# Performance work log

Hardware: AMD Instinct MI355X
Metric: run time of the kernel (lower is better)

Reference implementation:

```python
import jax, jax.numpy as jnp
import numpy as np
from jax import lax

D_MODEL = 96; D_STATE = 16; D_INNER = 192; DT_RANK = 6; K = 4
BSZ = 2; HH = 64; WW = 64


def setup_inputs() -> dict:
    key = jax.random.key(0)
    ks = jax.random.split(key, 16)
    f = lambda k, shape, s=0.02: (jax.random.normal(k, shape) * s).astype(jnp.float32)
    P = DT_RANK + 2 * D_STATE
    return {
        "x": jax.random.normal(ks[0], (BSZ, HH, WW, D_MODEL), jnp.float32),
        "W_in": f(ks[1], (2 * D_INNER, D_MODEL)),
        "b_in": jnp.zeros((2 * D_INNER,), jnp.float32),
        "conv_w": f(ks[2], (D_INNER, 1, 3, 3)),
        "conv_b": jnp.zeros((D_INNER,), jnp.float32),
        "W_xp": f(ks[3], (K * P, K * D_INNER)),
        "b_xp": jnp.zeros((K * P,), jnp.float32),
        "W_dt": f(ks[4], (K * D_INNER, K * DT_RANK)),
        "b_dt": f(ks[5], (K * D_INNER,), 0.1),
        "A_log": jax.random.normal(ks[6], (K * D_INNER, D_STATE), jnp.float32),
        "D_skip": jnp.ones((K * D_INNER,), jnp.float32),
        "dt_bias": jax.random.normal(ks[7], (K * D_INNER,), jnp.float32),
        "W_out": f(ks[8], (D_MODEL, D_INNER)),
        "b_out": jnp.zeros((D_MODEL,), jnp.float32),
        "gamma": jnp.ones((D_INNER,), jnp.float32),
        "beta": jnp.zeros((D_INNER,), jnp.float32),
    }


def cross_scan(x):
    # x: (B, D, H, W) -> (B, 4, D, L); dirs: row-major, col-major, and their reverses
    B, D, H, W = x.shape
    L = H * W
    x0 = x.reshape(B, D, L)
    x1 = jnp.swapaxes(x, 2, 3).reshape(B, D, L)
    return jnp.stack([x0, x1, x0[..., ::-1], x1[..., ::-1]], axis=1)


def cross_merge(ys):
    # ys: (B, 4, D, H, W) -> (B, D, L); inverse of cross_scan, summed
    B, Kk, D, H, W = ys.shape
    L = H * W
    yf = ys.reshape(B, Kk, D, L)
    y02 = yf[:, 0] + yf[:, 2, :, ::-1]
    y13 = yf[:, 1] + yf[:, 3, :, ::-1]
    y13 = jnp.swapaxes(y13.reshape(B, D, W, H), 2, 3).reshape(B, D, L)
    return y02 + y13


def selective_scan(u, dt, A, Bm, Cm, D_skip, dt_bias):
    # u, dt: (B,K,Dv,L); A: (K,Dv,N); Bm, Cm: (B,K,N,L); D_skip, dt_bias: (K,Dv)
    # NOTE: torch code repeats Bm/Cm across Dv; we broadcast instead (same math).
    dt = jax.nn.softplus(dt + dt_bias[None, :, :, None])
    dt_l = jnp.moveaxis(dt, -1, 0)   # (L,B,K,Dv)
    u_l = jnp.moveaxis(u, -1, 0)     # (L,B,K,Dv)
    B_l = jnp.moveaxis(Bm, -1, 0)    # (L,B,K,N)
    C_l = jnp.moveaxis(Cm, -1, 0)    # (L,B,K,N)

    def step(h, inp):
        dt_t, u_t, b_t, c_t = inp
        dA = jnp.exp(dt_t[..., None] * A[None])                 # (B,K,Dv,N)
        dBu = (dt_t * u_t)[..., None] * b_t[:, :, None, :]      # (B,K,Dv,N)
        h = dA * h + dBu
        y = jnp.einsum('bkdn,bkn->bkd', h, c_t)
        return h, y

    h0 = jnp.zeros(u.shape[:3] + (A.shape[-1],), u.dtype)
    _, ys = lax.scan(step, h0, (dt_l, u_l, B_l, C_l))
    ys = jnp.moveaxis(ys, 0, -1)  # (B,K,Dv,L)
    return ys + u * D_skip[None, :, :, None]


def reference(x, W_in, b_in, conv_w, conv_b, W_xp, b_xp, W_dt, b_dt,
              A_log, D_skip, dt_bias, W_out, b_out, gamma, beta):
    B, H, W, _ = x.shape
    L = H * W
    xz = x @ W_in.T + b_in
    xx, z = jnp.split(xz, 2, axis=-1)
    z = jax.nn.silu(z)
    xc = jnp.transpose(xx, (0, 3, 1, 2))  # (B, D, H, W)
    xc = lax.conv_general_dilated(xc, conv_w, (1, 1), 'SAME',
                                  feature_group_count=D_INNER,
                                  dimension_numbers=('NCHW', 'OIHW', 'NCHW'))
    xc = jax.nn.silu(xc + conv_b[None, :, None, None])

    xs = cross_scan(xc)                      # (B, K, D, L)
    xs_flat = xs.reshape(B, K * D_INNER, L)

    x_dbl = jnp.einsum('bcl,pc->bpl', xs_flat, W_xp) + b_xp[None, :, None]
    x_dbl = x_dbl.reshape(B, K, DT_RANK + 2 * D_STATE, L)
    dts, Bm, Cm = jnp.split(x_dbl, [DT_RANK, DT_RANK + D_STATE], axis=2)
    dts = dts.reshape(B, K * DT_RANK, L)
    dts = jnp.einsum('brl,dr->bdl', dts, W_dt) + b_dt[None, :, None]

    A = -jnp.exp(A_log).reshape(K, D_INNER, D_STATE)
    u = xs_flat.reshape(B, K, D_INNER, L)
    dt = dts.reshape(B, K, D_INNER, L)
    ys = selective_scan(u, dt, A, Bm, Cm,
                        D_skip.reshape(K, D_INNER), dt_bias.reshape(K, D_INNER))

    y = cross_merge(ys.reshape(B, K, D_INNER, H, W))  # (B, D, L)
    y = jnp.transpose(y.reshape(B, D_INNER, H, W), (0, 2, 3, 1))

    mu = jnp.mean(y, axis=-1, keepdims=True)
    var = jnp.mean(jnp.square(y - mu), axis=-1, keepdims=True)
    y = (y - mu) * lax.rsqrt(var + 1e-5) * gamma + beta
    y = y * z
    return y @ W_out.T + b_out
```

## Files before the change

### kernel.cpp

```cpp
#include <hip/hip_runtime.h>
#include <cstdint>
#include <cstddef>


#define CHUNK 32
#define NCK   128

#if __has_builtin(__builtin_amdgcn_exp2f)
#define EXP2(x) __builtin_amdgcn_exp2f(x)
#else
#define EXP2(x) exp2f(x)
#endif
#define LOG2E 1.44269504088896340736f

typedef __attribute__((ext_vector_type(8))) short short8;
typedef __attribute__((ext_vector_type(8))) unsigned short ushort8;
typedef __attribute__((ext_vector_type(4))) float f32x4;

__device__ __forceinline__ float siluf(float x){ return x * (1.f/(1.f+__expf(-x))); }
__device__ __forceinline__ unsigned short f2b(float f){
  uint32_t u = __float_as_uint(f);
  uint32_t r = (u + 0x7fffu + ((u>>16)&1u)) >> 16;
  return (unsigned short)r;
}

template<int KD, int STRA, int STRB>
__device__ __forceinline__ void micro_mm_T(const float (&As)[64][STRA], const float (&BsT)[KD][STRB],
                                           int tx, int ty, float (&acc)[4][4])
{
#pragma unroll 2
  for (int k4 = 0; k4 < KD/4; k4++){
    float a[4][4];
#pragma unroll
    for (int i = 0; i < 4; i++){
      float4 t = *(const float4*)&As[ty*4+i][k4*4];
      a[i][0]=t.x; a[i][1]=t.y; a[i][2]=t.z; a[i][3]=t.w;
    }
#pragma unroll
    for (int e = 0; e < 4; e++){
      float4 b = *(const float4*)&BsT[k4*4+e][tx*4];
#pragma unroll
      for (int i = 0; i < 4; i++){
        acc[i][0] = fmaf(a[i][e], b.x, acc[i][0]);
        acc[i][1] = fmaf(a[i][e], b.y, acc[i][1]);
        acc[i][2] = fmaf(a[i][e], b.z, acc[i][2]);
        acc[i][3] = fmaf(a[i][e], b.w, acc[i][3]);
      }
    }
  }
}

__global__ __launch_bounds__(256) void k_cast_w(
    const float* __restrict__ Wxp, unsigned short* __restrict__ Wf)
{
  int tid = blockIdx.x*256 + threadIdx.x;
  if (tid >= 18432) return;
  int lane = tid & 63; int rest = tid >> 6;
  int pt = rest % 6; rest /= 6;
  int k32 = rest & 3; rest >>= 2;
  int kc = rest % 6; int ph = rest / 6;
  int n = lane & 15, q = lane >> 4;
  int p = ph*96 + pt*16 + n;
  int kbase = kc*128 + k32*32 + q*8;
  unsigned short v[8];
#pragma unroll
  for (int j = 0; j < 8; j++)
    v[j] = (p < 152) ? f2b(Wxp[(size_t)p*768 + kbase + j]) : (unsigned short)0;
  *(ushort8*)(Wf + (size_t)tid*8) = *(ushort8*)v;
}

__global__ __launch_bounds__(256) void k_gemm_in(
    const float* __restrict__ x, const float* __restrict__ W,
    const float* __restrict__ bias, float* __restrict__ xx, float* __restrict__ zs)
{
  __shared__ float As[64][100];
  __shared__ float BsT[96][68];
  const int m0 = blockIdx.x*64, n0 = blockIdx.y*64;
  const int tid = threadIdx.x;
#pragma unroll
  for (int i = 0; i < 6; i++){
    int idx = tid + i*256;
    { int r = idx/24, c4 = idx%24;
      *(float4*)&As[r][c4*4] = *(const float4*)(x + (size_t)(m0+r)*96 + c4*4); }
    { int r = idx & 63, c4 = idx >> 6;
      float4 wv = *(const float4*)(W + (size_t)(n0+r)*96 + c4*4);
      BsT[c4*4+0][r]=wv.x; BsT[c4*4+1][r]=wv.y; BsT[c4*4+2][r]=wv.z; BsT[c4*4+3][r]=wv.w; }
  }
  __syncthreads();
  const int tx = tid & 15, ty = tid >> 4;
  float acc[4][4] = {};
  micro_mm_T<96,100,68>(As, BsT, tx, ty, acc);
#pragma unroll
  for (int i = 0; i < 4; i++){
    int m = m0 + ty*4 + i;
#pragma unroll
    for (int j = 0; j < 4; j++){
      int n = n0 + tx*4 + j;
      float v = acc[i][j] + bias[n];
      if (n < 192) xx[(size_t)m*192 + n] = v;
      else         zs[(size_t)m*192 + (n-192)] = siluf(v);
    }
  }
}

__global__ __launch_bounds__(256) void k_conv(
    const float* __restrict__ xx, const float* __restrict__ cw, const float* __restrict__ cb,
    float* __restrict__ xc, float* __restrict__ xcT,
    unsigned short* __restrict__ xcb, unsigned short* __restrict__ xcTb)
{
  int gid = blockIdx.x*256 + threadIdx.x;
  int c = gid % 192;
  int l = (gid/192) & 4095;
  int b = gid / (192*4096);
  int h = l >> 6, w = l & 63;
  float s = 0.f;
#pragma unroll
  for (int kh = 0; kh < 3; kh++){
    int h2 = h + kh - 1;
    if ((unsigned)h2 >= 64u) continue;
#pragma unroll
    for (int kw = 0; kw < 3; kw++){
      int w2 = w + kw - 1;
      if ((unsigned)w2 >= 64u) continue;
      s += xx[((size_t)b*4096 + h2*64 + w2)*192 + c] * cw[c*9 + kh*3 + kw];
    }
  }
  s = siluf(s + cb[c]);
  unsigned short sb = f2b(s);
  size_t i0 = ((size_t)b*4096 + l)*192 + c;
  xc[i0] = s; xcb[i0] = sb;
  int tl = (l & 63)*64 + (l >> 6);
  size_t i1 = ((size_t)b*4096 + tl)*192 + c;
  xcT[i1] = s; xcTb[i1] = sb;
}

__global__ __launch_bounds__(256) void k_gemm_xdbl(
    const unsigned short* __restrict__ xcb, const unsigned short* __restrict__ xcTb,
    const unsigned short* __restrict__ Wf, const float* __restrict__ bxp,
    float* __restrict__ xdbl)
{
  __shared__ unsigned short Bsh[4*6*64*8];
  const int tid = threadIdx.x;
  const int lane = tid & 63, w = tid >> 6;
  const int wl = w & 1, wp = w >> 1;
  const int l0 = blockIdx.x*64, ph = blockIdx.y, b = blockIdx.z;
  const int n = lane & 15, q = lane >> 4;
  f32x4 acc[2][3] = {};
  const unsigned short* slab0 = Wf + (size_t)ph*6*12288;
  for (int kc = 0; kc < 6; kc++){
    __syncthreads();
    const ushort8* srcp = (const ushort8*)(slab0 + (size_t)kc*12288);
#pragma unroll
    for (int t = 0; t < 6; t++) ((ushort8*)Bsh)[tid + t*256] = srcp[tid + t*256];
    __syncthreads();
#pragma unroll
    for (int k32 = 0; k32 < 4; k32++){
      int kk = kc*128 + k32*32;
      int dir = kk/192; int ch = kk%192 + q*8;
      const unsigned short* sp = (dir & 1) ? xcTb : xcb;
      bool rev = (dir >= 2);
      short8 a[2];
#pragma unroll
      for (int mt = 0; mt < 2; mt++){
        int ls = l0 + wl*32 + mt*16 + n;
        int row = rev ? 4095 - ls : ls;
        a[mt] = *(const short8*)(sp + ((size_t)b*4096 + row)*192 + ch);
      }
#pragma unroll
      for (int j = 0; j < 3; j++){
        short8 bfr = *(const short8*)&Bsh[((size_t)(k32*6 + wp*3 + j)*64 + lane)*8];
#pragma unroll
        for (int mt = 0; mt < 2; mt++)
          acc[mt][j] = __builtin_amdgcn_mfma_f32_16x16x32_bf16(a[mt], bfr, acc[mt][j], 0, 0, 0);
      }
    }
  }
#pragma unroll
  for (int mt = 0; mt < 2; mt++)
#pragma unroll
    for (int j = 0; j < 3; j++){
      int p = ph*96 + (wp*3+j)*16 + n;
      if (p < 152){
        int k = p/38, pp = p%38;
        int off = (pp < 6) ? pp : pp + 2;
        float bias = bxp[p];
#pragma unroll
        for (int reg = 0; reg < 4; reg++){
          int l = l0 + wl*32 + mt*16 + q*4 + reg;
          xdbl[(((size_t)b*4 + k)*4096 + l)*48 + off] = acc[mt][j][reg] + bias;
        }
      }
    }
}

__global__ __launch_bounds__(256) void k_gemm_dt(
    const float* __restrict__ xdbl, const float* __restrict__ Wdt,
    const float* __restrict__ bdt, const float* __restrict__ dtbias,
    float* __restrict__ dte)
{
  __shared__ float As[64][28];
  __shared__ float BsT[24][68];
  const int m0 = blockIdx.x*64;
  const int n0 = blockIdx.y*64;
  const int b  = blockIdx.z;
  const int tid = threadIdx.x;
#pragma unroll
  for (int i = 0; i < 6; i++){
    int idx = tid + i*256;
    { int r = idx/24, cc = idx%24;
      int kp = cc/6, ri = cc%6;
      As[r][cc] = xdbl[(((size_t)b*4 + kp)*4096 + (m0+r))*48 + ri]; }
    { int r = idx & 63, cc = idx >> 6;
      BsT[cc][r] = Wdt[(size_t)(n0+r)*24 + cc]; }
  }
  __syncthreads();
  const int tx = tid & 15, ty = tid >> 4;
  float acc[4][4] = {};
  micro_mm_T<24,28,68>(As, BsT, tx, ty, acc);
#pragma unroll
  for (int i = 0; i < 4; i++){
    int l = m0 + ty*4 + i;
#pragma unroll
    for (int j = 0; j < 4; j++){
      int c = n0 + tx*4 + j;
      float v = acc[i][j] + bdt[c] + dtbias[c];
      v = (v > 20.f) ? v : log1pf(__expf(v));
      dte[(((size_t)b*4 + c/192)*4096 + l)*192 + (c%192)] = v;
    }
  }
}

__global__ __launch_bounds__(256) void k_scanA(
    const float* __restrict__ xc, const float* __restrict__ xcT,
    const float* __restrict__ xdbl, const float* __restrict__ dte,
    const float* __restrict__ A_log,
    float* __restrict__ Pb, float* __restrict__ Sb)
{
  const int lane = threadIdx.x & 63;
  const int wid  = __builtin_amdgcn_readfirstlane(blockIdx.x*4 + (threadIdx.x >> 6));
  const int ck = wid & (NCK-1); const int g = wid / NCK;
  const int dblk = g % 3; const int bk = g / 3;
  const int k = bk & 3; const int b = bk >> 2;
  const int d = dblk*64 + lane; const int ch = k*192 + d;
  float An[16];
  {
    const float4* ap = (const float4*)(A_log + (size_t)ch*16);
#pragma unroll
    for (int i = 0; i < 4; i++){
      float4 t = ap[i];
      An[4*i+0] = -LOG2E*__expf(t.x); An[4*i+1] = -LOG2E*__expf(t.y);
      An[4*i+2] = -LOG2E*__expf(t.z); An[4*i+3] = -LOG2E*__expf(t.w);
    }
  }
  const int l0 = ck*CHUNK;
  const bool rev = (k >= 2);
  const float* srcb = (k & 1) ? xcT : xc;
  const float* dtp = dte  + (((size_t)b*4 + k)*4096 + l0)*192 + d;
  const float* xdp = xdbl + (((size_t)b*4 + k)*4096 + l0)*48;
  const float* up  = srcb + ((size_t)b*4096 + (rev ? 4095 - l0 : l0))*192 + d;
  const int ust = rev ? -192 : 192;
  float h[16];
#pragma unroll
  for (int n = 0; n < 16; n++) h[n] = 0.f;
  float sdt = 0.f;
#pragma unroll 2
  for (int t = 0; t < CHUNK; t++){
    float dt = dtp[0];
    float u  = up[0];
    float4 B0 = *(const float4*)(xdp + 8);
    float4 B1 = *(const float4*)(xdp + 12);
    float4 B2 = *(const float4*)(xdp + 16);
    float4 B3 = *(const float4*)(xdp + 20);
    float Bv[16] = {B0.x,B0.y,B0.z,B0.w, B1.x,B1.y,B1.z,B1.w,
                    B2.x,B2.y,B2.z,B2.w, B3.x,B3.y,B3.z,B3.w};
    float dtu = dt*u;
    sdt += dt;
#pragma unroll
    for (int n = 0; n < 16; n++){
      float dA = EXP2(dt*An[n]);
      h[n] = fmaf(dA, h[n], dtu*Bv[n]);
    }
    dtp += 192; xdp += 48; up += ust;
  }
  size_t base = ((size_t)wid*16)*64 + lane;
#pragma unroll
  for (int n = 0; n < 16; n++){
    Pb[base + n*64] = EXP2(An[n]*sdt);
    Sb[base + n*64] = h[n];
  }
}

__global__ __launch_bounds__(256) void k_scanB(
    const float* __restrict__ Pb, float* SbH0)
{
  int tid = blockIdx.x*256 + threadIdx.x;
  int lane = tid & 63; int n = (tid >> 6) & 15; int g = tid >> 10;
  float h = 0.f;
  for (int ck = 0; ck < NCK; ck++){
    size_t idx = (((size_t)(g*NCK + ck)*16) + n)*64 + lane;
    float p = Pb[idx];
    float s = SbH0[idx];
    SbH0[idx] = h;
    h = fmaf(p, h, s);
  }
}

__global__ __launch_bounds__(256) void k_scanC(
    const float* __restrict__ xc, const float* __restrict__ xcT,
    const float* __restrict__ xdbl, const float* __restrict__ dte,
    const float* __restrict__ A_log, const float* __restrict__ Dskip,
    const float* __restrict__ H0, float* __restrict__ ys)
{
  const int lane = threadIdx.x & 63;
  const int wid  = __builtin_amdgcn_readfirstlane(blockIdx.x*4 + (threadIdx.x >> 6));
  const int ck = wid & (NCK-1); const int g = wid / NCK;
  const int dblk = g % 3; const int bk = g / 3;
  const int k = bk & 3; const int b = bk >> 2;
  const int d = dblk*64 + lane; const int ch = k*192 + d;
  float An[16];
  {
    const float4* ap = (const float4*)(A_log + (size_t)ch*16);
#pragma unroll
    for (int i = 0; i < 4; i++){
      float4 t = ap[i];
      An[4*i+0] = -LOG2E*__expf(t.x); An[4*i+1] = -LOG2E*__expf(t.y);
      An[4*i+2] = -LOG2E*__expf(t.z); An[4*i+3] = -LOG2E*__expf(t.w);
    }
  }
  const float Dv = Dskip[ch];
  const int l0 = ck*CHUNK;
  const bool rev = (k >= 2);
  const float* srcb = (k & 1) ? xcT : xc;
  const float* dtp = dte  + (((size_t)b*4 + k)*4096 + l0)*192 + d;
  const float* xdp = xdbl + (((size_t)b*4 + k)*4096 + l0)*48;
  const float* up  = srcb + ((size_t)b*4096 + (rev ? 4095 - l0 : l0))*192 + d;
  const int ust = rev ? -192 : 192;
  float* ysb = ys + ((size_t)(k*2 + b))*4096*192 + d;
  float h[16];
  size_t base = ((size_t)wid*16)*64 + lane;
#pragma unroll
  for (int n = 0; n < 16; n++) h[n] = H0[base + n*64];
#pragma unroll 2
  for (int t = 0; t < CHUNK; t++){
    int l = l0 + t;
    float dt = dtp[0];
    float u  = up[0];
    float4 B0 = *(const float4*)(xdp + 8);
    float4 B1 = *(const float4*)(xdp + 12);
    float4 B2 = *(const float4*)(xdp + 16);
    float4 B3 = *(const float4*)(xdp + 20);
    float4 C0 = *(const float4*)(xdp + 24);
    float4 C1 = *(const float4*)(xdp + 28);
    float4 C2 = *(const float4*)(xdp + 32);
    float4 C3 = *(const float4*)(xdp + 36);
    float Bv[16] = {B0.x,B0.y,B0.z,B0.w, B1.x,B1.y,B1.z,B1.w,
                    B2.x,B2.y,B2.z,B2.w, B3.x,B3.y,B3.z,B3.w};
    float Cv[16] = {C0.x,C0.y,C0.z,C0.w, C1.x,C1.y,C1.z,C1.w,
                    C2.x,C2.y,C2.z,C2.w, C3.x,C3.y,C3.z,C3.w};
    float dtu = dt*u;
    float y = u*Dv;
#pragma unroll
    for (int n = 0; n < 16; n++){
      float dA = EXP2(dt*An[n]);
      h[n] = fmaf(dA, h[n], dtu*Bv[n]);
      y = fmaf(h[n], Cv[n], y);
    }
    int pos;
    if (k == 0)      pos = l;
    else if (k == 1) pos = (l & 63)*64 + (l >> 6);
    else { int l2 = 4095 - l; pos = (k == 2) ? l2 : ((l2 & 63)*64 + (l2 >> 6)); }
    ysb[(size_t)pos*192] = y;
    dtp += 192; xdp += 48; up += ust;
  }
}

__global__ __launch_bounds__(256) void k_ln(
    const float* __restrict__ ys, const float* __restrict__ zs,
    const float* __restrict__ gamma, const float* __restrict__ beta,
    float* __restrict__ yln)
{
  int row = blockIdx.x*4 + (threadIdx.x >> 6);
  int lane = threadIdx.x & 63;
  int b = row >> 12; int l = row & 4095;
  float v[3];
#pragma unroll
  for (int j = 0; j < 3; j++){
    int c = lane + j*64;
    float s = 0.f;
#pragma unroll
    for (int k = 0; k < 4; k++) s += ys[(((size_t)k*2 + b)*4096 + l)*192 + c];
    v[j] = s;
  }
  float tot = v[0] + v[1] + v[2];
#pragma unroll
  for (int o = 1; o < 64; o <<= 1) tot += __shfl_xor(tot, o);
  float mean = tot * (1.f/192.f);
  float d0 = v[0]-mean, d1 = v[1]-mean, d2 = v[2]-mean;
  float vs = d0*d0 + d1*d1 + d2*d2;
#pragma unroll
  for (int o = 1; o < 64; o <<= 1) vs += __shfl_xor(vs, o);
  float rstd = rsqrtf(vs*(1.f/192.f) + 1e-5f);
  float nd[3] = {d0, d1, d2};
#pragma unroll
  for (int j = 0; j < 3; j++){
    int c = lane + j*64;
    float val = nd[j]*rstd*gamma[c] + beta[c];
    val *= zs[(size_t)row*192 + c];
    yln[(size_t)row*192 + c] = val;
  }
}

__global__ __launch_bounds__(256) void k_gemm_out(
    const float* __restrict__ yln, const float* __restrict__ Wout,
    const float* __restrict__ bout, float* __restrict__ out)
{
  __shared__ float As[64][100];
  __shared__ float BsT[96][68];
  const int m0 = blockIdx.x*64, n0 = blockIdx.y*64;
  const int tid = threadIdx.x;
  const int tx = tid & 15, ty = tid >> 4;
  float acc[4][4] = {};
  for (int kc = 0; kc < 2; kc++){
    __syncthreads();
#pragma unroll
    for (int i = 0; i < 6; i++){
      int idx = tid + i*256;
      { int r = idx/24, c4 = idx%24;
        *(float4*)&As[r][c4*4] = *(const float4*)(yln + (size_t)(m0+r)*192 + kc*96 + c4*4); }
      { int r = idx & 63, c4 = idx >> 6;
        int nn = n0 + r;
        float4 wv = make_float4(0.f,0.f,0.f,0.f);
        if (nn < 96) wv = *(const float4*)(Wout + (size_t)nn*192 + kc*96 + c4*4);
        BsT[c4*4+0][r]=wv.x; BsT[c4*4+1][r]=wv.y; BsT[c4*4+2][r]=wv.z; BsT[c4*4+3][r]=wv.w; }
    }
    __syncthreads();
    micro_mm_T<96,100,68>(As, BsT, tx, ty, acc);
  }
#pragma unroll
  for (int i = 0; i < 4; i++){
    int m = m0 + ty*4 + i;
#pragma unroll
    for (int j = 0; j < 4; j++){
      int n = n0 + tx*4 + j;
      if (n < 96) out[(size_t)m*96 + n] = acc[i][j] + bout[n];
    }
  }
}

extern "C" void kernel_launch(void* const* d_in, const int* in_sizes, int n_in,
                              void* d_out, int out_size, void* d_ws, size_t ws_size,
                              hipStream_t stream)
{
  const float* x      = (const float*)d_in[0];
  const float* W_in   = (const float*)d_in[1];
  const float* b_in   = (const float*)d_in[2];
  const float* conv_w = (const float*)d_in[3];
  const float* conv_b = (const float*)d_in[4];
  const float* W_xp   = (const float*)d_in[5];
  const float* b_xp   = (const float*)d_in[6];
  const float* W_dt   = (const float*)d_in[7];
  const float* b_dt   = (const float*)d_in[8];
  const float* A_log  = (const float*)d_in[9];
  const float* D_skip = (const float*)d_in[10];
  const float* dt_bias= (const float*)d_in[11];
  const float* W_out  = (const float*)d_in[12];
  const float* b_out  = (const float*)d_in[13];
  const float* gamma  = (const float*)d_in[14];
  const float* beta   = (const float*)d_in[15];
  float* out = (float*)d_out;

  float* ws   = (float*)d_ws;
  float* xx   = ws;
  float* yln  = ws + 1572864;
  float* zs   = ws + 3145728;
  float* xc   = ws + 4718592;
  float* xcT  = ws + 6291456;
  float* xdbl = ws + 7864320;
  float* dte  = ws + 9437184;
  float* ysb  = ws + 15728640;
  float* SbH0 = xx;
  float* Pb   = ysb;
  unsigned short* xcb  = (unsigned short*)(ysb + 3145728);
  unsigned short* xcTb = xcb + 1572864;
  unsigned short* Wf   = (unsigned short*)(ysb + 4718592 + 786432);

  k_cast_w   <<<72,              256, 0, stream>>>(W_xp, Wf);
  k_gemm_in  <<<dim3(128, 6),    256, 0, stream>>>(x, W_in, b_in, xx, zs);
  k_conv     <<<6144,            256, 0, stream>>>(xx, conv_w, conv_b, xc, xcT, xcb, xcTb);
  k_gemm_xdbl<<<dim3(64, 2, 2),  256, 0, stream>>>(xcb, xcTb, Wf, b_xp, xdbl);
  k_gemm_dt  <<<dim3(64, 12, 2), 256, 0, stream>>>(xdbl, W_dt, b_dt, dt_bias, dte);
  k_scanA    <<<768,             256, 0, stream>>>(xc, xcT, xdbl, dte, A_log, Pb, SbH0);
  k_scanB    <<<96,              256, 0, stream>>>(Pb, SbH0);
  k_scanC    <<<768,             256, 0, stream>>>(xc, xcT, xdbl, dte, A_log, D_skip, SbH0, ysb);
  k_ln       <<<2048,            256, 0, stream>>>(ysb, zs, gamma, beta, yln);
  k_gemm_out <<<dim3(128, 2),    256, 0, stream>>>(yln, W_out, b_out, out);
}
```

Baseline: 238.4 us.

## Fuse dt projection and softplus into scan kernels, drop transposed fp32 copy

Removes the separate dt GEMM kernel and its large dte buffer. Both scan passes now compute dt per timestep from the 24 low-rank xdbl values and per-channel weights held in registers, then apply softplus. The transposed fp32 activation copy is dropped, and the scans index the original xc with a direction-dependent stride, writing outputs directly at merged positions. Scan B gets separate Pb/Sb/H0 buffers and loop unrolling. In exchange, the dt projection is recomputed in both scanA and scanC, and the column-direction reads and writes are now strided.

```diff
diff --git a/kernel.cpp b/kernel.cpp
--- a/kernel.cpp
+++ b/kernel.cpp
@@ -12,12 +12,16 @@
 #define EXP2(x) exp2f(x)
 #endif
 #define LOG2E 1.44269504088896340736f
+#define KSTRIDE 196608
 
 typedef __attribute__((ext_vector_type(8))) short short8;
 typedef __attribute__((ext_vector_type(8))) unsigned short ushort8;
 typedef __attribute__((ext_vector_type(4))) float f32x4;
 
 __device__ __forceinline__ float siluf(float x){ return x * (1.f/(1.f+__expf(-x))); }
+__device__ __forceinline__ float softplusf(float v){
+  return (v > 20.f) ? v : log1pf(__expf(v));
+}
 __device__ __forceinline__ unsigned short f2b(float f){
   uint32_t u = __float_as_uint(f);
   uint32_t r = (u + 0x7fffu + ((u>>16)&1u)) >> 16;
@@ -105,7 +109,7 @@
 
 __global__ __launch_bounds__(256) void k_conv(
     const float* __restrict__ xx, const float* __restrict__ cw, const float* __restrict__ cb,
-    float* __restrict__ xc, float* __restrict__ xcT,
+    float* __restrict__ xc,
     unsigned short* __restrict__ xcb, unsigned short* __restrict__ xcTb)
 {
   int gid = blockIdx.x*256 + threadIdx.x;
@@ -130,8 +134,7 @@
   size_t i0 = ((size_t)b*4096 + l)*192 + c;
   xc[i0] = s; xcb[i0] = sb;
   int tl = (l & 63)*64 + (l >> 6);
-  size_t i1 = ((size_t)b*4096 + tl)*192 + c;
-  xcT[i1] = s; xcTb[i1] = sb;
+  xcTb[((size_t)b*4096 + tl)*192 + c] = sb;
 }
 
 __global__ __launch_bounds__(256) void k_gemm_xdbl(
@@ -193,47 +196,10 @@
     }
 }
 
-__global__ __launch_bounds__(256) void k_gemm_dt(
-    const float* __restrict__ xdbl, const float* __restrict__ Wdt,
+__global__ __launch_bounds__(256) void k_scanA(
+    const float* __restrict__ xc, const float* __restrict__ xdbl,
+    const float* __restrict__ A_log, const float* __restrict__ Wdt,
     const float* __restrict__ bdt, const float* __restrict__ dtbias,
-    float* __restrict__ dte)
-{
-  __shared__ float As[64][28];
-  __shared__ float BsT[24][68];
-  const int m0 = blockIdx.x*64;
-  const int n0 = blockIdx.y*64;
-  const int b  = blockIdx.z;
-  const int tid = threadIdx.x;
-#pragma unroll
-  for (int i = 0; i < 6; i++){
-    int idx = tid + i*256;
-    { int r = idx/24, cc = idx%24;
-      int kp = cc/6, ri = cc%6;
-      As[r][cc] = xdbl[(((size_t)b*4 + kp)*4096 + (m0+r))*48 + ri]; }
-    { int r = idx & 63, cc = idx >> 6;
-      BsT[cc][r] = Wdt[(size_t)(n0+r)*24 + cc]; }
-  }
-  __syncthreads();
-  const int tx = tid & 15, ty = tid >> 4;
-  float acc[4][4] = {};
-  micro_mm_T<24,28,68>(As, BsT, tx, ty, acc);
-#pragma unroll
-  for (int i = 0; i < 4; i++){
-    int l = m0 + ty*4 + i;
-#pragma unroll
-    for (int j = 0; j < 4; j++){
-      int c = n0 + tx*4 + j;
-      float v = acc[i][j] + bdt[c] + dtbias[c];
-      v = (v > 20.f) ? v : log1pf(__expf(v));
-      dte[(((size_t)b*4 + c/192)*4096 + l)*192 + (c%192)] = v;
-    }
-  }
-}
-
-__global__ __launch_bounds__(256) void k_scanA(
-    const float* __restrict__ xc, const float* __restrict__ xcT,
-    const float* __restrict__ xdbl, const float* __restrict__ dte,
-    const float* __restrict__ A_log,
     float* __restrict__ Pb, float* __restrict__ Sb)
 {
   const int lane = threadIdx.x & 63;
@@ -252,27 +218,44 @@
       An[4*i+2] = -LOG2E*__expf(t.z); An[4*i+3] = -LOG2E*__expf(t.w);
     }
   }
+  float Wr[24];
+#pragma unroll
+  for (int r = 0; r < 24; r++) Wr[r] = Wdt[(size_t)ch*24 + r];
+  const float bsum = bdt[ch] + dtbias[ch];
   const int l0 = ck*CHUNK;
   const bool rev = (k >= 2);
-  const float* srcb = (k & 1) ? xcT : xc;
-  const float* dtp = dte  + (((size_t)b*4 + k)*4096 + l0)*192 + d;
-  const float* xdp = xdbl + (((size_t)b*4 + k)*4096 + l0)*48;
-  const float* up  = srcb + ((size_t)b*4096 + (rev ? 4095 - l0 : l0))*192 + d;
-  const int ust = rev ? -192 : 192;
+  const int tr = k & 1;
+  const int T0 = tr ? ((l0 & 63)*64 + (l0 >> 6)) : l0;
+  const int rs = tr ? 64 : 1;
+  const int row0 = rev ? 4095 - T0 : T0;
+  const int rstep = (rev ? -rs : rs)*192;
+  const float* up  = xc + ((size_t)b*4096 + row0)*192 + d;
+  const float* xq  = xdbl + ((size_t)b*4*4096 + l0)*48;
+  const float* xbc = xq + (size_t)k*KSTRIDE;
   float h[16];
 #pragma unroll
   for (int n = 0; n < 16; n++) h[n] = 0.f;
   float sdt = 0.f;
 #pragma unroll 2
   for (int t = 0; t < CHUNK; t++){
-    float dt = dtp[0];
     float u  = up[0];
-    float4 B0 = *(const float4*)(xdp + 8);
-    float4 B1 = *(const float4*)(xdp + 12);
-    float4 B2 = *(const float4*)(xdp + 16);
-    float4 B3 = *(const float4*)(xdp + 20);
+    float4 B0 = *(const float4*)(xbc + 8);
+    float4 B1 = *(const float4*)(xbc + 12);
+    float4 B2 = *(const float4*)(xbc + 16);
+    float4 B3 = *(const float4*)(xbc + 20);
     float Bv[16] = {B0.x,B0.y,B0.z,B0.w, B1.x,B1.y,B1.z,B1.w,
                     B2.x,B2.y,B2.z,B2.w, B3.x,B3.y,B3.z,B3.w};
+    float v = bsum;
+#pragma unroll
+    for (int kp = 0; kp < 4; kp++){
+      const float* qp = xq + (size_t)kp*KSTRIDE;
+      float4 a  = *(const float4*)(qp);
+      float2 b2 = *(const float2*)(qp + 4);
+      v = fmaf(Wr[kp*6+0], a.x, v);  v = fmaf(Wr[kp*6+1], a.y, v);
+      v = fmaf(Wr[kp*6+2], a.z, v);  v = fmaf(Wr[kp*6+3], a.w, v);
+      v = fmaf(Wr[kp*6+4], b2.x, v); v = fmaf(Wr[kp*6+5], b2.y, v);
+    }
+    float dt = softplusf(v);
     float dtu = dt*u;
     sdt += dt;
 #pragma unroll
@@ -280,7 +263,7 @@
       float dA = EXP2(dt*An[n]);
       h[n] = fmaf(dA, h[n], dtu*Bv[n]);
     }
-    dtp += 192; xdp += 48; up += ust;
+    xq += 48; xbc += 48; up += rstep;
   }
   size_t base = ((size_t)wid*16)*64 + lane;
 #pragma unroll
@@ -291,24 +274,24 @@
 }
 
 __global__ __launch_bounds__(256) void k_scanB(
-    const float* __restrict__ Pb, float* SbH0)
+    const float* __restrict__ Pb, const float* __restrict__ Sb, float* __restrict__ H0)
 {
   int tid = blockIdx.x*256 + threadIdx.x;
   int lane = tid & 63; int n = (tid >> 6) & 15; int g = tid >> 10;
   float h = 0.f;
+#pragma unroll 4
   for (int ck = 0; ck < NCK; ck++){
     size_t idx = (((size_t)(g*NCK + ck)*16) + n)*64 + lane;
-    float p = Pb[idx];
-    float s = SbH0[idx];
-    SbH0[idx] = h;
-    h = fmaf(p, h, s);
+    H0[idx] = h;
+    h = fmaf(Pb[idx], h, Sb[idx]);
   }
 }
 
 __global__ __launch_bounds__(256) void k_scanC(
-    const float* __restrict__ xc, const float* __restrict__ xcT,
-    const float* __restrict__ xdbl, const float* __restrict__ dte,
-    const float* __restrict__ A_log, const float* __restrict__ Dskip,
+    const float* __restrict__ xc, const float* __restrict__ xdbl,
+    const float* __restrict__ A_log, const float* __restrict__ Wdt,
+    const float* __restrict__ bdt, const float* __restrict__ dtbias,
+    const float* __restrict__ Dskip,
     const float* __restrict__ H0, float* __restrict__ ys)
 {
   const int lane = threadIdx.x & 63;
@@ -327,36 +310,52 @@
       An[4*i+2] = -LOG2E*__expf(t.z); An[4*i+3] = -LOG2E*__expf(t.w);
     }
   }
+  float Wr[24];
+#pragma unroll
+  for (int r = 0; r < 24; r++) Wr[r] = Wdt[(size_t)ch*24 + r];
+  const float bsum = bdt[ch] + dtbias[ch];
   const float Dv = Dskip[ch];
   const int l0 = ck*CHUNK;
   const bool rev = (k >= 2);
-  const float* srcb = (k & 1) ? xcT : xc;
-  const float* dtp = dte  + (((size_t)b*4 + k)*4096 + l0)*192 + d;
-  const float* xdp = xdbl + (((size_t)b*4 + k)*4096 + l0)*48;
-  const float* up  = srcb + ((size_t)b*4096 + (rev ? 4095 - l0 : l0))*192 + d;
-  const int ust = rev ? -192 : 192;
-  float* ysb = ys + ((size_t)(k*2 + b))*4096*192 + d;
+  const int tr = k & 1;
+  const int T0 = tr ? ((l0 & 63)*64 + (l0 >> 6)) : l0;
+  const int rs = tr ? 64 : 1;
+  const int row0 = rev ? 4095 - T0 : T0;
+  const int rstep = (rev ? -rs : rs)*192;
+  const float* up  = xc + ((size_t)b*4096 + row0)*192 + d;
+  const float* xq  = xdbl + ((size_t)b*4*4096 + l0)*48;
+  const float* xbc = xq + (size_t)k*KSTRIDE;
+  float* ysp = ys + ((size_t)(k*2 + b))*4096*192 + (size_t)row0*192 + d;
   float h[16];
   size_t base = ((size_t)wid*16)*64 + lane;
 #pragma unroll
   for (int n = 0; n < 16; n++) h[n] = H0[base + n*64];
 #pragma unroll 2
   for (int t = 0; t < CHUNK; t++){
-    int l = l0 + t;
-    float dt = dtp[0];
     float u  = up[0];
-    float4 B0 = *(const float4*)(xdp + 8);
-    float4 B1 = *(const float4*)(xdp + 12);
-    float4 B2 = *(const float4*)(xdp + 16);
-    float4 B3 = *(const float4*)(xdp + 20);
-    float4 C0 = *(const float4*)(xdp + 24);
-    float4 C1 = *(const float4*)(xdp + 28);
-    float4 C2 = *(const float4*)(xdp + 32);
-    float4 C3 = *(const float4*)(xdp + 36);
+    float4 B0 = *(const float4*)(xbc + 8);
+    float4 B1 = *(const float4*)(xbc + 12);
+    float4 B2 = *(const float4*)(xbc + 16);
+    float4 B3 = *(const float4*)(xbc + 20);
+    float4 C0 = *(const float4*)(xbc + 24);
+    float4 C1 = *(const float4*)(xbc + 28);
+    float4 C2 = *(const float4*)(xbc + 32);
+    float4 C3 = *(const float4*)(xbc + 36);
     float Bv[16] = {B0.x,B0.y,B0.z,B0.w, B1.x,B1.y,B1.z,B1.w,
                     B2.x,B2.y,B2.z,B2.w, B3.x,B3.y,B3.z,B3.w};
     float Cv[16] = {C0.x,C0.y,C0.z,C0.w, C1.x,C1.y,C1.z,C1.w,
                     C2.x,C2.y,C2.z,C2.w, C3.x,C3.y,C3.z,C3.w};
+    float v = bsum;
+#pragma unroll
+    for (int kp = 0; kp < 4; kp++){
+      const float* qp = xq + (size_t)kp*KSTRIDE;
+      float4 a  = *(const float4*)(qp);
+      float2 b2 = *(const float2*)(qp + 4);
+      v = fmaf(Wr[kp*6+0], a.x, v);  v = fmaf(Wr[kp*6+1], a.y, v);
+      v = fmaf(Wr[kp*6+2], a.z, v);  v = fmaf(Wr[kp*6+3], a.w, v);
+      v = fmaf(Wr[kp*6+4], b2.x, v); v = fmaf(Wr[kp*6+5], b2.y, v);
+    }
+    float dt = softplusf(v);
     float dtu = dt*u;
     float y = u*Dv;
 #pragma unroll
@@ -365,12 +364,8 @@
       h[n] = fmaf(dA, h[n], dtu*Bv[n]);
       y = fmaf(h[n], Cv[n], y);
     }
-    int pos;
-    if (k == 0)      pos = l;
-    else if (k == 1) pos = (l & 63)*64 + (l >> 6);
-    else { int l2 = 4095 - l; pos = (k == 2) ? l2 : ((l2 & 63)*64 + (l2 >> 6)); }
-    ysb[(size_t)pos*192] = y;
-    dtp += 192; xdp += 48; up += ust;
+    ysp[0] = y;
+    xq += 48; xbc += 48; up += rstep; ysp += rstep;
   }
 }
 
@@ -471,27 +466,25 @@
 
   float* ws   = (float*)d_ws;
   float* xx   = ws;
-  float* yln  = ws + 1572864;
-  float* zs   = ws + 3145728;
-  float* xc   = ws + 4718592;
-  float* xcT  = ws + 6291456;
-  float* xdbl = ws + 7864320;
-  float* dte  = ws + 9437184;
-  float* ysb  = ws + 15728640;
-  float* SbH0 = xx;
-  float* Pb   = ysb;
-  unsigned short* xcb  = (unsigned short*)(ysb + 3145728);
+  float* zs   = ws + 1572864;
+  float* xc   = ws + 3145728;
+  float* xdbl = ws + 4718592;
+  float* ysb  = ws + 6291456;
+  float* yln  = ws + 12582912;
+  float* Pb   = ws + 14155776;
+  float* Sb   = ws + 17301504;
+  float* H0   = ws + 20447232;
+  unsigned short* xcb  = (unsigned short*)(ws + 23592960);
   unsigned short* xcTb = xcb + 1572864;
-  unsigned short* Wf   = (unsigned short*)(ysb + 4718592 + 786432);
-
-  k_cast_w   <<<72,              256, 0, stream>>>(W_xp, Wf);
-  k_gemm_in  <<<dim3(128, 6),    256, 0, stream>>>(x, W_in, b_in, xx, zs);
-  k_conv     <<<6144,            256, 0, stream>>>(xx, conv_w, conv_b, xc, xcT, xcb, xcTb);
-  k_gemm_xdbl<<<dim3(64, 2, 2),  256, 0, stream>>>(xcb, xcTb, Wf, b_xp, xdbl);
-  k_gemm_dt  <<<dim3(64, 12, 2), 256, 0, stream>>>(xdbl, W_dt, b_dt, dt_bias, dte);
-  k_scanA    <<<768,             256, 0, stream>>>(xc, xcT, xdbl, dte, A_log, Pb, SbH0);
-  k_scanB    <<<96,              256, 0, stream>>>(Pb, SbH0);
-  k_scanC    <<<768,             256, 0, stream>>>(xc, xcT, xdbl, dte, A_log, D_skip, SbH0, ysb);
-  k_ln       <<<2048,            256, 0, stream>>>(ysb, zs, gamma, beta, yln);
-  k_gemm_out <<<dim3(128, 2),    256, 0, stream>>>(yln, W_out, b_out, out);
-}
+  unsigned short* Wf   = (unsigned short*)(ws + 25165824);
+
+  k_cast_w   <<<72,             256, 0, stream>>>(W_xp, Wf);
+  k_gemm_in  <<<dim3(128, 6),   256, 0, stream>>>(x, W_in, b_in, xx, zs);
+  k_conv     <<<6144,           256, 0, stream>>>(xx, conv_w, conv_b, xc, xcb, xcTb);
+  k_gemm_xdbl<<<dim3(64, 2, 2), 256, 0, stream>>>(xcb, xcTb, Wf, b_xp, xdbl);
+  k_scanA    <<<768,            256, 0, stream>>>(xc, xdbl, A_log, W_dt, b_dt, dt_bias, Pb, Sb);
+  k_scanB    <<<96,             256, 0, stream>>>(Pb, Sb, H0);
+  k_scanC    <<<768,            256, 0, stream>>>(xc, xdbl, A_log, W_dt, b_dt, dt_bias, D_skip, H0, ysb);
+  k_ln       <<<2048,           256, 0, stream>>>(ysb, zs, gamma, beta, yln);
+  k_gemm_out <<<dim3(128, 2),   256, 0, stream>>>(yln, W_out, b_out, out);
+}
```

After: 266.7 us. 1.12x slower.
